# Performance work log

Hardware: AMD Instinct MI355X
Metric: run time of the kernel (lower is better)

The kernel has to match this reference:

```python
import jax, jax.numpy as jnp
import numpy as np

B, T, C, H = 4, 1024, 1024, 16
HS = C // H  # head_size = 64
EPS = 1e-5


def layer_norm(x, w, b):
    mu = jnp.mean(x, axis=-1, keepdims=True)
    var = jnp.mean(jnp.square(x - mu), axis=-1, keepdims=True)
    return (x - mu) * jax.lax.rsqrt(var + EPS) * w + b


def setup_inputs() -> dict:
    key = jax.random.key(0)
    ks = jax.random.split(key, 12)
    s = 0.02
    return {
        "x": jax.random.normal(ks[0], (B, T, C), jnp.float32),
        "ln1_w": jnp.ones((C,), jnp.float32),
        "ln1_b": jnp.zeros((C,), jnp.float32),
        "Wk": jax.random.normal(ks[1], (H, C, HS), jnp.float32) * s,
        "Wq": jax.random.normal(ks[2], (H, C, HS), jnp.float32) * s,
        "Wv": jax.random.normal(ks[3], (H, C, HS), jnp.float32) * s,
        "Wo": jax.random.normal(ks[4], (C, C), jnp.float32) * s,
        "bo": jnp.zeros((C,), jnp.float32),
        "ln2_w": jnp.ones((C,), jnp.float32),
        "ln2_b": jnp.zeros((C,), jnp.float32),
        "W1": jax.random.normal(ks[5], (C, 4 * C), jnp.float32) * s,
        "b1": jnp.zeros((4 * C,), jnp.float32),
        "prelu_a": jnp.asarray(0.25, jnp.float32),
        "W2": jax.random.normal(ks[6], (4 * C, C), jnp.float32) * s,
        "b2": jnp.zeros((C,), jnp.float32),
    }


def reference(x, ln1_w, ln1_b, Wk, Wq, Wv, Wo, bo, ln2_w, ln2_b, W1, b1, prelu_a, W2, b2):
    # --- self-attention branch (pre-LN) ---
    h = layer_norm(x, ln1_w, ln1_b)  # [B,T,C]
    k = jnp.einsum('btc,hcd->bhtd', h, Wk)
    q = jnp.einsum('btc,hcd->bhtd', h, Wq)
    v = jnp.einsum('btc,hcd->bhtd', h, Wv)
    # NOTE: source computes k @ q^T (not q @ k^T) scaled by n_embd**-0.5
    wei = jnp.einsum('bhtd,bhsd->bhts', k, q) * (C ** -0.5)  # [B,H,T,T]
    causal = jnp.tril(jnp.ones((T, T), bool))
    wei = jnp.where(causal, wei, -jnp.inf)
    wei = jax.nn.softmax(wei, axis=-1)
    out = jnp.einsum('bhts,bhsd->bthd', wei, v).reshape(B, T, C)
    out = out @ Wo + bo
    x = x + out
    # --- feed-forward branch (pre-LN) ---
    h2 = layer_norm(x, ln2_w, ln2_b)
    f = h2 @ W1 + b1
    f = jnp.where(f > 0, f, prelu_a * f)  # PReLU, single scalar param
    f = f @ W2 + b2
    return x + f
```

## Files before the change

### kernel.cpp

```cpp
#include <hip/hip_runtime.h>


typedef __bf16 bf16_t;
typedef __attribute__((ext_vector_type(8))) __bf16 bfx8;
typedef __attribute__((ext_vector_type(4))) __bf16 bfx4;
typedef __attribute__((ext_vector_type(4))) float f32x4;
typedef __attribute__((ext_vector_type(8))) unsigned short u16x8;
typedef unsigned int u32;

#define MFMA_BF16(a, b, c) __builtin_amdgcn_mfma_f32_16x16x32_bf16((a), (b), (c), 0, 0, 0)
#define GLOAD_LDS16(g, l)                                                     \
  __builtin_amdgcn_global_load_lds((__attribute__((address_space(1))) void*)(g), \
                                   (__attribute__((address_space(3))) void*)(l), 16, 0, 0)
#define BARX()                      \
  __builtin_amdgcn_s_barrier();     \
  __builtin_amdgcn_sched_barrier(0)
#define VMW6()                                     \
  asm volatile("s_waitcnt vmcnt(6)" ::: "memory"); \
  __builtin_amdgcn_sched_barrier(0)
#define VMW0()                                     \
  asm volatile("s_waitcnt vmcnt(0)" ::: "memory"); \
  __builtin_amdgcn_sched_barrier(0)

__global__ __launch_bounds__(256) void ln_kernel(const float* __restrict__ x,
                                                 const float* __restrict__ w,
                                                 const float* __restrict__ b,
                                                 bf16_t* __restrict__ out) {
  const int row = blockIdx.x;
  const int tid = threadIdx.x;
  const float4 v = reinterpret_cast<const float4*>(x + (size_t)row * 1024)[tid];
  float s = v.x + v.y + v.z + v.w;
  float s2 = v.x * v.x + v.y * v.y + v.z * v.z + v.w * v.w;
#pragma unroll
  for (int off = 1; off < 64; off <<= 1) {
    s += __shfl_xor(s, off);
    s2 += __shfl_xor(s2, off);
  }
  __shared__ float red[8];
  const int wv = tid >> 6;
  if ((tid & 63) == 0) {
    red[wv] = s;
    red[4 + wv] = s2;
  }
  __syncthreads();
  s = red[0] + red[1] + red[2] + red[3];
  s2 = red[4] + red[5] + red[6] + red[7];
  const float mu = s * (1.0f / 1024.0f);
  const float rs = rsqrtf(s2 * (1.0f / 1024.0f) - mu * mu + 1e-5f);
  const float4 wv4 = reinterpret_cast<const float4*>(w)[tid];
  const float4 bv4 = reinterpret_cast<const float4*>(b)[tid];
  bfx4 o;
  o[0] = (bf16_t)((v.x - mu) * rs * wv4.x + bv4.x);
  o[1] = (bf16_t)((v.y - mu) * rs * wv4.y + bv4.y);
  o[2] = (bf16_t)((v.z - mu) * rs * wv4.z + bv4.z);
  o[3] = (bf16_t)((v.w - mu) * rs * wv4.w + bv4.w);
  reinterpret_cast<bfx4*>(out + (size_t)row * 1024)[tid] = o;
}

__device__ __forceinline__ void tc_body(const float* __restrict__ in,
                                        bf16_t* __restrict__ out, int K, int N, int k0,
                                        int n0, float (*tile)[65], int t) {
  const int rl = t >> 4, cl = (t & 15) * 4;
#pragma unroll
  for (int p = 0; p < 4; ++p) {
    const int r = p * 16 + rl;
    const float4 v = *reinterpret_cast<const float4*>(in + (size_t)(k0 + r) * N + n0 + cl);
    tile[r][cl] = v.x;
    tile[r][cl + 1] = v.y;
    tile[r][cl + 2] = v.z;
    tile[r][cl + 3] = v.w;
  }
  __syncthreads();
#pragma unroll
  for (int p = 0; p < 2; ++p) {
    const int idx = p * 256 + t;
    const int n = idx >> 3, kc = (idx & 7) * 8;
    bfx8 o;
#pragma unroll
    for (int i = 0; i < 8; ++i) o[i] = (bf16_t)tile[kc + i][n];
    *reinterpret_cast<bfx8*>(out + (size_t)(n0 + n) * K + k0 + kc) = o;
  }
}

__global__ __launch_bounds__(256) void transpose_cast(const float* __restrict__ in,
                                                      bf16_t* __restrict__ out, int K,
                                                      int N) {
  __shared__ float tile[64][65];
  tc_body(in, out, K, N, blockIdx.x * 64, blockIdx.y * 64, tile, threadIdx.x);
}

__global__ __launch_bounds__(256) void transpose_qkv(const float* __restrict__ Wq,
                                                     const float* __restrict__ Wk,
                                                     const float* __restrict__ Wv,
                                                     bf16_t* __restrict__ out) {
  __shared__ float tile[64][65];
  const int z = blockIdx.y;
  const int sel = z >> 4, h = z & 15;
  const float* in = ((sel == 0) ? Wq : (sel == 1) ? Wk : Wv) + h * 65536;
  bf16_t* o = out + (size_t)sel * 1048576 + h * 65536;
  tc_body(in, o, 1024, 64, blockIdx.x * 64, 0, tile, threadIdx.x);
}

enum { EPI_QKV = 0, EPI_WO = 1 };

template <int EPI, int BM, int BN, int NT>
__global__ __launch_bounds__(NT, 2) void gemm_bt(
    const bf16_t* __restrict__ A, const bf16_t* __restrict__ BT,
    const float* __restrict__ bias, const float* __restrict__ res,
    float* __restrict__ outf, bf16_t* __restrict__ ob0, bf16_t* __restrict__ ob1,
    bf16_t* __restrict__ ob2, int K, int N) {
  constexpr int WM = 2;
  constexpr int WN = NT / 64 / WM;
  constexpr int MF = BM / WM / 16;
  constexpr int NF = BN / WN / 16;
  constexpr int ACH = BM * 64 / (NT * 8);
  constexpr int BCH = BN * 64 / (NT * 8);
  constexpr int LOADS = ACH + BCH;
  static_assert(LOADS == 8 || LOADS == 6, "add a vmcnt case");
  __shared__ __align__(16) bf16_t sA[2][BM * 64];
  __shared__ __align__(16) bf16_t sB[2][BN * 64];
  const int tid = threadIdx.x;
  const int lane = tid & 63;
  const int w = tid >> 6;
  const int wr = w / WN, wc = w % WN;
  const int g = lane >> 4, l15 = lane & 15;
  const int row0 = blockIdx.x * BM, col0 = blockIdx.y * BN;
  const int rowbase = row0 + wr * (BM / WM);
  const int colbase = wc * (BN / WN);

  f32x4 acc[MF][NF] = {};

  auto stage = [&](int k0, int buf) {
#pragma unroll
    for (int j = 0; j < ACH; ++j) {
      const int chunk = j * NT + tid;
      const int r = chunk >> 3, c = chunk & 7;
      GLOAD_LDS16(A + (size_t)(row0 + r) * K + k0 + ((c ^ (r & 7)) * 8),
                  sA[buf] + chunk * 8);
    }
#pragma unroll
    for (int j = 0; j < BCH; ++j) {
      const int chunk = j * NT + tid;
      const int r = chunk >> 3, c = chunk & 7;
      GLOAD_LDS16(BT + (size_t)(col0 + r) * K + k0 + ((c ^ (r & 7)) * 8),
                  sB[buf] + chunk * 8);
    }
  };

  stage(0, 0);
  const int nk = K >> 6;
  for (int t = 0; t < nk; ++t) {
    const int cur = t & 1;
    if (t + 1 < nk) {
      stage((t + 1) << 6, cur ^ 1);
      __builtin_amdgcn_sched_barrier(0);
      if constexpr (LOADS == 8)
        asm volatile("s_waitcnt vmcnt(8)" ::: "memory");
      else
        asm volatile("s_waitcnt vmcnt(6)" ::: "memory");
    } else {
      __builtin_amdgcn_sched_barrier(0);
      asm volatile("s_waitcnt vmcnt(0)" ::: "memory");
    }
    __builtin_amdgcn_s_barrier();
    __builtin_amdgcn_sched_barrier(0);
    const bf16_t* __restrict__ pA = sA[cur];
    const bf16_t* __restrict__ pB = sB[cur];
#pragma unroll
    for (int kk = 0; kk < 2; ++kk) {
      bfx8 af[MF], bfr[NF];
#pragma unroll
      for (int m = 0; m < MF; ++m) {
        const int r = wr * (BM / WM) + m * 16 + l15;
        const int c = (kk * 4 + g) ^ (r & 7);
        af[m] = *reinterpret_cast<const bfx8*>(pA + r * 64 + c * 8);
      }
#pragma unroll
      for (int n = 0; n < NF; ++n) {
        const int r = colbase + n * 16 + l15;
        const int c = (kk * 4 + g) ^ (r & 7);
        bfr[n] = *reinterpret_cast<const bfx8*>(pB + r * 64 + c * 8);
      }
#pragma unroll
      for (int m = 0; m < MF; ++m)
#pragma unroll
        for (int n = 0; n < NF; ++n) acc[m][n] = MFMA_BF16(af[m], bfr[n], acc[m][n]);
    }
    __builtin_amdgcn_sched_barrier(0);
    __builtin_amdgcn_s_barrier();
  }

#pragma unroll
  for (int m = 0; m < MF; ++m) {
#pragma unroll
    for (int n = 0; n < NF; ++n) {
#pragma unroll
      for (int j = 0; j < 4; ++j) {
        const int row = rowbase + m * 16 + (g << 2) + j;
        const int col = col0 + colbase + n * 16 + l15;
        const float v = acc[m][n][j];
        if (EPI == EPI_QKV) {
          const int sel = col >> 10;
          const int h = (col >> 6) & 15, d = col & 63;
          const int bb = row >> 10, t = row & 1023;
          bf16_t* dst = (sel == 0) ? ob0 : (sel == 1) ? ob1 : ob2;
          dst[((size_t)(bb * 16 + h) * 1024 + t) * 64 + d] = (bf16_t)v;
        } else {
          outf[(size_t)row * N + col] = v + bias[col] + res[(size_t)row * N + col];
        }
      }
    }
  }
}

__device__ __forceinline__ void stageA8(const bf16_t* __restrict__ A, int Ks, int row0,
                                        int k0, int mh, bf16_t* dst, int tid) {
#pragma unroll
  for (int g2 = 0; g2 < 2; ++g2) {
    const int band = g2 * 128 + mh * 64;
    const int row = band + (tid >> 3);
    GLOAD_LDS16(A + (size_t)(row0 + row) * Ks + k0 + (((tid & 7) ^ (row & 7)) * 8),
                dst + band * 64 + tid * 8);
  }
}

__device__ __forceinline__ void stageB8(const bf16_t* __restrict__ BT, int Ks, int col0,
                                        int k0, int nh, bf16_t* dst, int tid) {
#pragma unroll
  for (int g2 = 0; g2 < 2; ++g2) {
    const int rho = g2 * 64 + (tid >> 3);
    const int grow = (rho >> 5) * 64 + nh * 32 + (rho & 31);
    GLOAD_LDS16(BT + (size_t)(col0 + grow) * Ks + k0 + (((tid & 7) ^ (rho & 7)) * 8),
                dst + nh * 8192 + g2 * 4096 + tid * 8);
  }
}

template <int MH, int NH, bool LOADA>
__device__ __forceinline__ void quad8(const bf16_t* __restrict__ pA,
                                      const bf16_t* __restrict__ pB, int wr, int wc,
                                      int l15, int g, bfx8 (&af)[4][2],
                                      f32x4 (&acc)[8][4]) {
  if (LOADA) {
#pragma unroll
    for (int i = 0; i < 4; ++i) {
      const int r = wr * 128 + (MH * 4 + i) * 16 + l15;
#pragma unroll
      for (int kk = 0; kk < 2; ++kk)
        af[i][kk] =
            *reinterpret_cast<const bfx8*>(pA + r * 64 + (((kk * 4 + g) ^ (r & 7)) * 8));
    }
  }
  bfx8 bfr[2][2];
#pragma unroll
  for (int i = 0; i < 2; ++i) {
    const int rho = wc * 32 + i * 16 + l15;
#pragma unroll
    for (int kk = 0; kk < 2; ++kk)
      bfr[i][kk] = *reinterpret_cast<const bfx8*>(pB + NH * 8192 + rho * 64 +
                                                  (((kk * 4 + g) ^ (rho & 7)) * 8));
  }
  __builtin_amdgcn_s_setprio(1);
#pragma unroll
  for (int i = 0; i < 4; ++i)
#pragma unroll
    for (int jn = 0; jn < 2; ++jn)
#pragma unroll
      for (int kk = 0; kk < 2; ++kk)
        acc[MH * 4 + i][NH * 2 + jn] =
            MFMA_BF16(af[i][kk], bfr[jn][kk], acc[MH * 4 + i][NH * 2 + jn]);
  __builtin_amdgcn_s_setprio(0);
}

template <bool PRELU>
__global__ __launch_bounds__(512, 2) void gemm_8ph(
    const bf16_t* __restrict__ A, const bf16_t* __restrict__ BT,
    const float* __restrict__ bias, const float* __restrict__ prelu,
    bf16_t* __restrict__ outb, int Ks, int Klen, int N, size_t zstride) {
  __shared__ __align__(16) bf16_t sA[2][256 * 64];
  __shared__ __align__(16) bf16_t sB[2][256 * 64];
  const int tid = threadIdx.x;
  const int lane = tid & 63;
  const int w = tid >> 6;
  const int wr = w >> 2, wc = w & 3;
  const int g = lane >> 4, l15 = lane & 15;
  const int row0 = blockIdx.x * 256, col0 = blockIdx.y * 256;
  const int koff = blockIdx.z * Klen;

  f32x4 acc[8][4] = {};
  bfx8 af[4][2];

  stageA8(A, Ks, row0, koff, 0, sA[0], tid);
  stageB8(BT, Ks, col0, koff, 0, sB[0], tid);
  stageB8(BT, Ks, col0, koff, 1, sB[0], tid);
  stageA8(A, Ks, row0, koff, 1, sA[0], tid);
  stageA8(A, Ks, row0, koff + 64, 0, sA[1], tid);
  stageB8(BT, Ks, col0, koff + 64, 0, sB[1], tid);

  const int nt = Klen >> 7;
  for (int j = 0; j < nt; ++j) {
    const bool more = (j + 1 < nt);
    const int ku1 = koff + ((2 * j + 1) << 6), k2 = koff + ((2 * j + 2) << 6),
              k3 = koff + ((2 * j + 3) << 6);
    BARX();
    stageB8(BT, Ks, col0, ku1, 1, sB[1], tid);
    VMW6();
    BARX();
    quad8<0, 0, true>(sA[0], sB[0], wr, wc, l15, g, af, acc);
    BARX();
    stageA8(A, Ks, row0, ku1, 1, sA[1], tid);
    quad8<0, 1, false>(sA[0], sB[0], wr, wc, l15, g, af, acc);
    BARX();
    if (more) stageA8(A, Ks, row0, k2, 0, sA[0], tid);
    quad8<1, 0, true>(sA[0], sB[0], wr, wc, l15, g, af, acc);
    BARX();
    if (more) stageB8(BT, Ks, col0, k2, 0, sB[0], tid);
    quad8<1, 1, false>(sA[0], sB[0], wr, wc, l15, g, af, acc);
    BARX();
    if (more) {
      stageB8(BT, Ks, col0, k2, 1, sB[0], tid);
      VMW6();
    } else {
      VMW0();
    }
    BARX();
    quad8<0, 0, true>(sA[1], sB[1], wr, wc, l15, g, af, acc);
    BARX();
    if (more) stageA8(A, Ks, row0, k2, 1, sA[0], tid);
    quad8<0, 1, false>(sA[1], sB[1], wr, wc, l15, g, af, acc);
    BARX();
    if (more) stageA8(A, Ks, row0, k3, 0, sA[1], tid);
    quad8<1, 0, true>(sA[1], sB[1], wr, wc, l15, g, af, acc);
    BARX();
    if (more) stageB8(BT, Ks, col0, k3, 0, sB[1], tid);
    quad8<1, 1, false>(sA[1], sB[1], wr, wc, l15, g, af, acc);
  }

  bf16_t* o = outb + (size_t)blockIdx.z * zstride;
  const float pa = PRELU ? prelu[0] : 0.0f;
#pragma unroll
  for (int m = 0; m < 8; ++m) {
#pragma unroll
    for (int n = 0; n < 4; ++n) {
#pragma unroll
      for (int j = 0; j < 4; ++j) {
        const int row = row0 + wr * 128 + m * 16 + (g << 2) + j;
        const int col = col0 + wc * 64 + n * 16 + l15;
        float t = acc[m][n][j];
        if (PRELU) {
          t += bias[col];
          t = (t > 0.0f) ? t : pa * t;
        }
        o[(size_t)row * N + col] = (bf16_t)t;
      }
    }
  }
}

__global__ __launch_bounds__(256) void reduce_mlp2(const bf16_t* __restrict__ part,
                                                   const float* __restrict__ b2,
                                                   float* __restrict__ out) {
  const int idx = (blockIdx.x * 256 + threadIdx.x) * 8;
  const int col = idx & 1023;
  float a[8];
  {
    const float4 o0 = *reinterpret_cast<const float4*>(out + idx);
    const float4 o1 = *reinterpret_cast<const float4*>(out + idx + 4);
    const float4 b0 = *reinterpret_cast<const float4*>(b2 + col);
    const float4 b1 = *reinterpret_cast<const float4*>(b2 + col + 4);
    a[0] = o0.x + b0.x; a[1] = o0.y + b0.y; a[2] = o0.z + b0.z; a[3] = o0.w + b0.w;
    a[4] = o1.x + b1.x; a[5] = o1.y + b1.y; a[6] = o1.z + b1.z; a[7] = o1.w + b1.w;
  }
#pragma unroll
  for (int s = 0; s < 4; ++s) {
    const u16x8 p = *reinterpret_cast<const u16x8*>(part + (size_t)s * 4194304 + idx);
#pragma unroll
    for (int i = 0; i < 8; ++i) a[i] += __uint_as_float((u32)p[i] << 16);
  }
  float4 r0{a[0], a[1], a[2], a[3]}, r1{a[4], a[5], a[6], a[7]};
  *reinterpret_cast<float4*>(out + idx) = r0;
  *reinterpret_cast<float4*>(out + idx + 4) = r1;
}

__global__ __launch_bounds__(256) void attn_kernel(const bf16_t* __restrict__ kproj,
                                                   const bf16_t* __restrict__ qproj,
                                                   const bf16_t* __restrict__ vproj,
                                                   bf16_t* __restrict__ att) {
  __shared__ __align__(16) bf16_t sK[2][64 * 64];
  __shared__ __align__(16) bf16_t sVt[2][64 * 64];
  __shared__ __align__(16) bf16_t sP[4][16 * 64];
  const int tid = threadIdx.x, lane = tid & 63, w = tid >> 6;
  const int g = lane >> 4, l15 = lane & 15;
  const int f = blockIdx.x;
  const int tb = 15 - ((f >> 3) >> 3);
  const int bh = (((f >> 3) & 7) << 3) + (f & 7);
  const size_t head = (size_t)bh * (1024 * 64);
  const int b = bh >> 4, h = bh & 15;
  const int vrow = 2 * (tid >> 3);
  const int vdb = tid & 7;
  const int t0 = tb * 64;
  const int nsb = tb + 1;

  bfx8 aq0, aq1;
  {
    const bf16_t* qrow = kproj + head + (size_t)(t0 + w * 16 + l15) * 64 + g * 8;
    aq0 = *reinterpret_cast<const bfx8*>(qrow);
    aq1 = *reinterpret_cast<const bfx8*>(qrow + 32);
  }

  {
#pragma unroll
    for (int j = 0; j < 2; ++j) {
      const int chunk = j * 256 + tid;
      const int r = chunk >> 3, c = chunk & 7;
      const int cs = c ^ (r & 7);
      GLOAD_LDS16(qproj + head + (size_t)r * 64 + cs * 8, sK[0] + chunk * 8);
    }
    const bf16_t* vp = vproj + head + (size_t)vrow * 64 + vdb * 8;
    const u16x8 v0 = *reinterpret_cast<const u16x8*>(vp);
    const u16x8 v1 = *reinterpret_cast<const u16x8*>(vp + 64);
#pragma unroll
    for (int i = 0; i < 8; ++i) {
      const int d = vdb * 8 + i;
      const int cc = ((vrow >> 3) ^ i ^ vdb) & 7;
      const u32 pk = ((u32)v1[i] << 16) | (u32)v0[i];
      *reinterpret_cast<u32*>(sVt[0] + d * 64 + cc * 8 + (vrow & 7)) = pk;
    }
  }
  __syncthreads();

  f32x4 accO[4] = {};
  float m2[4], lp[4];
#pragma unroll
  for (int j = 0; j < 4; ++j) {
    m2[j] = -1e30f;
    lp[j] = 0.0f;
  }

  for (int sb = 0; sb < nsb; ++sb) {
    const int cur = sb & 1;
    const bool pf = (sb + 1 < nsb);
    const bool diag = (sb == tb);
    u16x8 v0n, v1n;
    if (pf) {
      const int s0n = (sb + 1) * 64;
#pragma unroll
      for (int j = 0; j < 2; ++j) {
        const int chunk = j * 256 + tid;
        const int r = chunk >> 3, c = chunk & 7;
        const int cs = c ^ (r & 7);
        GLOAD_LDS16(qproj + head + (size_t)(s0n + r) * 64 + cs * 8, sK[cur ^ 1] + chunk * 8);
      }
      const bf16_t* vp = vproj + head + (size_t)(s0n + vrow) * 64 + vdb * 8;
      v0n = *reinterpret_cast<const u16x8*>(vp);
      v1n = *reinterpret_cast<const u16x8*>(vp + 64);
    }

    f32x4 accS[4] = {};
    const bf16_t* sKc = sK[cur];
#pragma unroll
    for (int kk = 0; kk < 2; ++kk) {
      const bfx8 aq = kk ? aq1 : aq0;
#pragma unroll
      for (int n = 0; n < 4; ++n) {
        const int r = n * 16 + l15;
        const int c = (kk * 4 + g) ^ (r & 7);
        const bfx8 bk = *reinterpret_cast<const bfx8*>(sKc + r * 64 + c * 8);
        accS[n] = MFMA_BF16(aq, bk, accS[n]);
      }
    }

    constexpr float SC = 0.04508056640625f;
    const int rbase = t0 + w * 16 + (g << 2);
    const int cbase = sb * 64 + l15;
    float rmx[4];
    float dmax = -3e38f;
#pragma unroll
    for (int j = 0; j < 4; ++j) {
      const int t = rbase + j;
      float mx = -1e30f;
      if (diag) {
#pragma unroll
        for (int n = 0; n < 4; ++n) {
          float v = accS[n][j] * SC;
          v = ((cbase + n * 16) <= t) ? v : -1e30f;
          accS[n][j] = v;
          mx = fmaxf(mx, v);
        }
      } else {
#pragma unroll
        for (int n = 0; n < 4; ++n) {
          const float v = accS[n][j] * SC;
          accS[n][j] = v;
          mx = fmaxf(mx, v);
        }
      }
      rmx[j] = mx;
      dmax = fmaxf(dmax, mx - m2[j]);
    }
    if (__any(dmax > 8.0f)) {
#pragma unroll
      for (int j = 0; j < 4; ++j) {
        float mx = rmx[j];
        mx = fmaxf(mx, __shfl_xor(mx, 1));
        mx = fmaxf(mx, __shfl_xor(mx, 2));
        mx = fmaxf(mx, __shfl_xor(mx, 4));
        mx = fmaxf(mx, __shfl_xor(mx, 8));
        const float mnew = fmaxf(m2[j], mx);
        const float al = __builtin_amdgcn_exp2f(m2[j] - mnew);
        m2[j] = mnew;
        lp[j] *= al;
#pragma unroll
        for (int n = 0; n < 4; ++n) accO[n][j] *= al;
      }
    }
#pragma unroll
    for (int j = 0; j < 4; ++j) {
      float s = 0.0f;
#pragma unroll
      for (int n = 0; n < 4; ++n) {
        const float p = __builtin_amdgcn_exp2f(accS[n][j] - m2[j]);
        accS[n][j] = p;
        s += p;
      }
      lp[j] += s;
    }

    bf16_t* sPw = sP[w];
#pragma unroll
    for (int n = 0; n < 4; ++n)
#pragma unroll
      for (int j = 0; j < 4; ++j) {
        const int r = (g << 2) + j;
        const int s = n * 16 + l15;
        const int cc = (s >> 3) ^ (r & 7);
        sPw[r * 64 + cc * 8 + (s & 7)] = (bf16_t)accS[n][j];
      }

    const bf16_t* sVc = sVt[cur];
#pragma unroll
    for (int kk = 0; kk < 2; ++kk) {
      bfx8 ap;
      {
        const int r = l15;
        const int c = (kk * 4 + g) ^ (r & 7);
        ap = *reinterpret_cast<const bfx8*>(sPw + r * 64 + c * 8);
      }
#pragma unroll
      for (int n = 0; n < 4; ++n) {
        const int d = n * 16 + l15;
        const int c = (kk * 4 + g) ^ (d & 7) ^ ((d >> 3) & 7);
        const bfx8 bv = *reinterpret_cast<const bfx8*>(sVc + d * 64 + c * 8);
        accO[n] = MFMA_BF16(ap, bv, accO[n]);
      }
    }

    if (pf) {
#pragma unroll
      for (int i = 0; i < 8; ++i) {
        const int d = vdb * 8 + i;
        const int cc = ((vrow >> 3) ^ i ^ vdb) & 7;
        const u32 pk = ((u32)v1n[i] << 16) | (u32)v0n[i];
        *reinterpret_cast<u32*>(sVt[cur ^ 1] + d * 64 + cc * 8 + (vrow & 7)) = pk;
      }
    }
    __syncthreads();
  }

#pragma unroll
  for (int j = 0; j < 4; ++j) {
    float l = lp[j];
    l += __shfl_xor(l, 1);
    l += __shfl_xor(l, 2);
    l += __shfl_xor(l, 4);
    l += __shfl_xor(l, 8);
    const float inv = 1.0f / l;
    const int t = t0 + w * 16 + (g << 2) + j;
#pragma unroll
    for (int n = 0; n < 4; ++n) {
      const int d = n * 16 + l15;
      att[((size_t)(b * 1024 + t)) * 1024 + h * 64 + d] = (bf16_t)(accO[n][j] * inv);
    }
  }
}

extern "C" void kernel_launch(void* const* d_in, const int* in_sizes, int n_in,
                              void* d_out, int out_size, void* d_ws, size_t ws_size,
                              hipStream_t stream) {
  (void)in_sizes; (void)n_in; (void)out_size; (void)ws_size;
  const float* x = (const float*)d_in[0];
  const float* ln1w = (const float*)d_in[1];
  const float* ln1b = (const float*)d_in[2];
  const float* Wk = (const float*)d_in[3];
  const float* Wq = (const float*)d_in[4];
  const float* Wv = (const float*)d_in[5];
  const float* Wo = (const float*)d_in[6];
  const float* bo = (const float*)d_in[7];
  const float* ln2w = (const float*)d_in[8];
  const float* ln2b = (const float*)d_in[9];
  const float* W1 = (const float*)d_in[10];
  const float* b1 = (const float*)d_in[11];
  const float* pa = (const float*)d_in[12];
  const float* W2 = (const float*)d_in[13];
  const float* b2 = (const float*)d_in[14];
  float* out = (float*)d_out;
  char* ws = (char*)d_ws;
  const size_t MB = 1ull << 20;
  bf16_t* h1 = (bf16_t*)(ws + 0 * MB);
  bf16_t* h2 = (bf16_t*)(ws + 8 * MB);
  bf16_t* qb = (bf16_t*)(ws + 16 * MB);
  bf16_t* kb = (bf16_t*)(ws + 24 * MB);
  bf16_t* vb = (bf16_t*)(ws + 32 * MB);
  bf16_t* attb = (bf16_t*)(ws + 40 * MB);
  bf16_t* fbuf = (bf16_t*)(ws + 48 * MB);
  bf16_t* part = (bf16_t*)(ws + 16 * MB);
  bf16_t* WqkvT = (bf16_t*)(ws + 80 * MB);
  bf16_t* WoT = (bf16_t*)(ws + 86 * MB);
  bf16_t* W1T = (bf16_t*)(ws + 88 * MB);
  bf16_t* W2T = (bf16_t*)(ws + 96 * MB);

  transpose_qkv<<<dim3(16, 48), 256, 0, stream>>>(Wq, Wk, Wv, WqkvT);
  transpose_cast<<<dim3(16, 16), 256, 0, stream>>>(Wo, WoT, 1024, 1024);
  transpose_cast<<<dim3(16, 64), 256, 0, stream>>>(W1, W1T, 1024, 4096);
  transpose_cast<<<dim3(64, 16), 256, 0, stream>>>(W2, W2T, 4096, 1024);

  ln_kernel<<<4096, 256, 0, stream>>>(x, ln1w, ln1b, h1);
  gemm_bt<EPI_QKV, 256, 256, 512><<<dim3(16, 12), 512, 0, stream>>>(
      h1, WqkvT, nullptr, nullptr, nullptr, qb, kb, vb, 1024, 3072);
  attn_kernel<<<1024, 256, 0, stream>>>(kb, qb, vb, attb);
  gemm_bt<EPI_WO, 64, 128, 256><<<dim3(64, 8), 256, 0, stream>>>(
      attb, WoT, bo, x, out, nullptr, nullptr, nullptr, 1024, 1024);
  ln_kernel<<<4096, 256, 0, stream>>>(out, ln2w, ln2b, h2);
  gemm_8ph<true><<<dim3(16, 16, 1), 512, 0, stream>>>(h2, W1T, b1, pa, fbuf, 1024, 1024,
                                                      4096, 0);
  gemm_8ph<false><<<dim3(16, 4, 4), 512, 0, stream>>>(fbuf, W2T, nullptr, nullptr, part,
                                                      4096, 1024, 1024, 4194304);
  reduce_mlp2<<<2048, 256, 0, stream>>>(part, b2, out);
}
```

Baseline: 204.5 us.

## Restructure 8-phase GEMM pipeline to issue LDS reads before prefetch and barrier

Splits the per-phase fragment load and MFMA block in the 256x256 GEMM into separate steps. Each phase now reads its LDS fragments, issues the next global-to-LDS prefetch, waits at a barrier, then runs the MFMAs and hits a second barrier. The vmcnt waits move to phase ends with a lower count (4), and the launch bound drops from 2 blocks per CU to 1. The goal is to hide LDS read latency under the barrier and prefetch issue and to free registers. The cost is lower occupancy and a different set of barriers that may serialize waves.

```diff
diff --git a/kernel.cpp b/kernel.cpp
--- a/kernel.cpp
+++ b/kernel.cpp
@@ -12,14 +12,9 @@
 #define GLOAD_LDS16(g, l)                                                     \
   __builtin_amdgcn_global_load_lds((__attribute__((address_space(1))) void*)(g), \
                                    (__attribute__((address_space(3))) void*)(l), 16, 0, 0)
-#define BARX()                      \
-  __builtin_amdgcn_s_barrier();     \
-  __builtin_amdgcn_sched_barrier(0)
-#define VMW6()                                     \
-  asm volatile("s_waitcnt vmcnt(6)" ::: "memory"); \
-  __builtin_amdgcn_sched_barrier(0)
-#define VMW0()                                     \
-  asm volatile("s_waitcnt vmcnt(0)" ::: "memory"); \
+#define SBAR() __builtin_amdgcn_sched_barrier(0)
+#define VMW(N)                                       \
+  asm volatile("s_waitcnt vmcnt(" #N ")" ::: "memory"); \
   __builtin_amdgcn_sched_barrier(0)
 
 __global__ __launch_bounds__(256) void ln_kernel(const float* __restrict__ x,
@@ -153,17 +148,17 @@
     const int cur = t & 1;
     if (t + 1 < nk) {
       stage((t + 1) << 6, cur ^ 1);
-      __builtin_amdgcn_sched_barrier(0);
+      SBAR();
       if constexpr (LOADS == 8)
         asm volatile("s_waitcnt vmcnt(8)" ::: "memory");
       else
         asm volatile("s_waitcnt vmcnt(6)" ::: "memory");
     } else {
-      __builtin_amdgcn_sched_barrier(0);
+      SBAR();
       asm volatile("s_waitcnt vmcnt(0)" ::: "memory");
     }
     __builtin_amdgcn_s_barrier();
-    __builtin_amdgcn_sched_barrier(0);
+    SBAR();
     const bf16_t* __restrict__ pA = sA[cur];
     const bf16_t* __restrict__ pB = sB[cur];
 #pragma unroll
@@ -186,7 +181,7 @@
 #pragma unroll
         for (int n = 0; n < NF; ++n) acc[m][n] = MFMA_BF16(af[m], bfr[n], acc[m][n]);
     }
-    __builtin_amdgcn_sched_barrier(0);
+    SBAR();
     __builtin_amdgcn_s_barrier();
   }
 
@@ -236,10 +231,10 @@
 }
 
 template <int MH, int NH, bool LOADA>
-__device__ __forceinline__ void quad8(const bf16_t* __restrict__ pA,
-                                      const bf16_t* __restrict__ pB, int wr, int wc,
-                                      int l15, int g, bfx8 (&af)[4][2],
-                                      f32x4 (&acc)[8][4]) {
+__device__ __forceinline__ void frag_read(const bf16_t* __restrict__ pA,
+                                          const bf16_t* __restrict__ pB, int wr, int wc,
+                                          int l15, int g, bfx8 (&af)[4][2],
+                                          bfx8 (&bfr)[2][2]) {
   if (LOADA) {
 #pragma unroll
     for (int i = 0; i < 4; ++i) {
@@ -250,7 +245,6 @@
             *reinterpret_cast<const bfx8*>(pA + r * 64 + (((kk * 4 + g) ^ (r & 7)) * 8));
     }
   }
-  bfx8 bfr[2][2];
 #pragma unroll
   for (int i = 0; i < 2; ++i) {
     const int rho = wc * 32 + i * 16 + l15;
@@ -259,6 +253,11 @@
       bfr[i][kk] = *reinterpret_cast<const bfx8*>(pB + NH * 8192 + rho * 64 +
                                                   (((kk * 4 + g) ^ (rho & 7)) * 8));
   }
+}
+
+template <int MH, int NH>
+__device__ __forceinline__ void frag_mma(const bfx8 (&af)[4][2], const bfx8 (&bfr)[2][2],
+                                         f32x4 (&acc)[8][4]) {
   __builtin_amdgcn_s_setprio(1);
 #pragma unroll
   for (int i = 0; i < 4; ++i)
@@ -271,8 +270,22 @@
   __builtin_amdgcn_s_setprio(0);
 }
 
+#define PH(MH, NH, LA, PAB, PBB, STAGE, WAITC)                  \
+  {                                                             \
+    bfx8 bfr[2][2];                                             \
+    frag_read<MH, NH, LA>(PAB, PBB, wr, wc, l15, g, af, bfr);   \
+    STAGE;                                                      \
+    WAITC;                                                      \
+    __builtin_amdgcn_s_barrier();                               \
+    asm volatile("s_waitcnt lgkmcnt(0)" ::: "memory");          \
+    SBAR();                                                     \
+    frag_mma<MH, NH>(af, bfr, acc);                             \
+    SBAR();                                                     \
+    __builtin_amdgcn_s_barrier();                               \
+  }
+
 template <bool PRELU>
-__global__ __launch_bounds__(512, 2) void gemm_8ph(
+__global__ __launch_bounds__(512, 1) void gemm_8ph(
     const bf16_t* __restrict__ A, const bf16_t* __restrict__ BT,
     const float* __restrict__ bias, const float* __restrict__ prelu,
     bf16_t* __restrict__ outb, int Ks, int Klen, int N, size_t zstride) {
@@ -295,44 +308,25 @@
   stageA8(A, Ks, row0, koff, 1, sA[0], tid);
   stageA8(A, Ks, row0, koff + 64, 0, sA[1], tid);
   stageB8(BT, Ks, col0, koff + 64, 0, sB[1], tid);
+  VMW(4);
+  __builtin_amdgcn_s_barrier();
 
   const int nt = Klen >> 7;
   for (int j = 0; j < nt; ++j) {
     const bool more = (j + 1 < nt);
-    const int ku1 = koff + ((2 * j + 1) << 6), k2 = koff + ((2 * j + 2) << 6),
-              k3 = koff + ((2 * j + 3) << 6);
-    BARX();
-    stageB8(BT, Ks, col0, ku1, 1, sB[1], tid);
-    VMW6();
-    BARX();
-    quad8<0, 0, true>(sA[0], sB[0], wr, wc, l15, g, af, acc);
-    BARX();
-    stageA8(A, Ks, row0, ku1, 1, sA[1], tid);
-    quad8<0, 1, false>(sA[0], sB[0], wr, wc, l15, g, af, acc);
-    BARX();
-    if (more) stageA8(A, Ks, row0, k2, 0, sA[0], tid);
-    quad8<1, 0, true>(sA[0], sB[0], wr, wc, l15, g, af, acc);
-    BARX();
-    if (more) stageB8(BT, Ks, col0, k2, 0, sB[0], tid);
-    quad8<1, 1, false>(sA[0], sB[0], wr, wc, l15, g, af, acc);
-    BARX();
-    if (more) {
-      stageB8(BT, Ks, col0, k2, 1, sB[0], tid);
-      VMW6();
-    } else {
-      VMW0();
-    }
-    BARX();
-    quad8<0, 0, true>(sA[1], sB[1], wr, wc, l15, g, af, acc);
-    BARX();
-    if (more) stageA8(A, Ks, row0, k2, 1, sA[0], tid);
-    quad8<0, 1, false>(sA[1], sB[1], wr, wc, l15, g, af, acc);
-    BARX();
-    if (more) stageA8(A, Ks, row0, k3, 0, sA[1], tid);
-    quad8<1, 0, true>(sA[1], sB[1], wr, wc, l15, g, af, acc);
-    BARX();
-    if (more) stageB8(BT, Ks, col0, k3, 0, sB[1], tid);
-    quad8<1, 1, false>(sA[1], sB[1], wr, wc, l15, g, af, acc);
+    const int ku1 = koff + ((2 * j + 1) << 6);
+    const int k2 = koff + ((2 * j + 2) << 6);
+    const int k3 = koff + ((2 * j + 3) << 6);
+    PH(0, 0, true,  sA[0], sB[0], stageB8(BT, Ks, col0, ku1, 1, sB[1], tid), );
+    PH(0, 1, false, sA[0], sB[0], stageA8(A, Ks, row0, ku1, 1, sA[1], tid), );
+    PH(1, 0, true,  sA[0], sB[0], if (more) stageA8(A, Ks, row0, k2, 0, sA[0], tid), );
+    PH(1, 1, false, sA[0], sB[0], if (more) stageB8(BT, Ks, col0, k2, 0, sB[0], tid),
+       if (more) { VMW(4); } else { VMW(0); });
+    PH(0, 0, true,  sA[1], sB[1], if (more) stageB8(BT, Ks, col0, k2, 1, sB[0], tid), );
+    PH(0, 1, false, sA[1], sB[1], if (more) stageA8(A, Ks, row0, k2, 1, sA[0], tid), );
+    PH(1, 0, true,  sA[1], sB[1], if (more) stageA8(A, Ks, row0, k3, 0, sA[1], tid), );
+    PH(1, 1, false, sA[1], sB[1], if (more) stageB8(BT, Ks, col0, k3, 0, sB[1], tid),
+       if (more) { VMW(4); });
   }
 
   bf16_t* o = outb + (size_t)blockIdx.z * zstride;
```

New measurement: 204.0 us. No clear change (-0.2%).
